# Performance work log

Hardware: AMD Instinct MI355X
Metric: run time of the kernel (lower is better)

Reference implementation:

```python
import jax, jax.numpy as jnp
import numpy as np

NPOINT = 2048

def setup_inputs() -> dict:
    key = jax.random.key(0)
    xyz = jax.random.normal(key, (32, 3, 65536), dtype=jnp.float32)
    return {"xyz": xyz}

def furthest_point_sampling(pts, npoint):
    # pts: [B, N, 3] -> indices [B, npoint] int32
    B, N, _ = pts.shape
    batch = jnp.arange(B)

    def step(carry, _):
        dist, farthest = carry  # dist [B,N], farthest [B]
        centroid = pts[batch, farthest]              # [B, 3]
        d = jnp.sum((pts - centroid[:, None, :]) ** 2, axis=-1)  # [B, N]
        dist = jnp.minimum(dist, d)
        nxt = jnp.argmax(dist, axis=-1).astype(jnp.int32)
        return (dist, nxt), farthest

    init = (jnp.full((B, N), 1e10, dtype=pts.dtype),
            jnp.zeros((B,), dtype=jnp.int32))
    _, idx = jax.lax.scan(step, init, None, length=npoint)
    return idx.T  # [B, npoint]

def reference(xyz):
    # xyz: [B, 3, N]; module permutes to [B, N, 3] and runs FPS
    pts = jnp.transpose(xyz, (0, 2, 1)).astype(jnp.float32)
    return furthest_point_sampling(pts, NPOINT)
```

## Files before the change

kernel.cpp:

```cpp
#include <hip/hip_runtime.h>
#include <stdint.h>

#pragma clang fp contract(off)

#define NPT      2048
#define NBATCH   32
#define NPTS     65536
#define MEMBERS  8
#define NTHREADS 512
#define CHUNK    (NPTS / MEMBERS)
#define PPT      (CHUNK / NTHREADS)
#define WPB      (NTHREADS / 64)
#define PADSLOTS 32

__device__ __forceinline__ uint32_t f2u(float f) { return __float_as_uint(f); }
__device__ __forceinline__ float u2f(uint32_t u) { return __uint_as_float(u); }

__device__ __forceinline__ void amerge(float& v, int& i, float ov, int oi) {
    if (ov > v || (ov == v && oi < i)) { v = ov; i = oi; }
}

template<int CTRL>
__device__ __forceinline__ void dpp_round(float& v, int& i) {
    float ov = u2f((uint32_t)__builtin_amdgcn_mov_dpp((int)f2u(v), CTRL, 0xf, 0xf, true));
    int   oi = __builtin_amdgcn_mov_dpp(i, CTRL, 0xf, 0xf, true);
    amerge(v, i, ov, oi);
}
__device__ __forceinline__ void swz16_round(float& v, int& i) {
    float ov = u2f((uint32_t)__builtin_amdgcn_ds_swizzle((int)f2u(v), 0x401F));
    int   oi = __builtin_amdgcn_ds_swizzle(i, 0x401F);
    amerge(v, i, ov, oi);
}
__device__ __forceinline__ void row16_argmax(float& v, int& i) {
    dpp_round<0xB1>(v, i);
    dpp_round<0x4E>(v, i);
    dpp_round<0x141>(v, i);
    dpp_round<0x140>(v, i);
}
__device__ __forceinline__ void oct_argmax(float& v, int& i) {
    dpp_round<0xB1>(v, i);
    dpp_round<0x4E>(v, i);
    dpp_round<0x141>(v, i);
}

__global__ void __launch_bounds__(NTHREADS)
fps_kernel(const float* __restrict__ xyz, int* __restrict__ out,
           uint64_t* __restrict__ cand)
{
    __shared__ float    sx[CHUNK];
    __shared__ uint64_t red[WPB * 4];
    __shared__ uint32_t bc[4];

    const int i = blockIdx.x;
    const int q = i >> 3;
    const int batch  = (i & 7) * 4 + (q & 3);
    const int member = q >> 2;
    const int tid  = threadIdx.x;
    const int lane = tid & 63;
    const int wv   = tid >> 6;

    const float* xb = xyz + (size_t)batch * 3 * NPTS;
    const int gbase = member * CHUNK;

    float py[PPT], pz[PPT], pd[PPT];
#pragma unroll
    for (int k = 0; k < PPT; ++k) {
        int p = tid + k * NTHREADS;
        int g = gbase + p;
        sx[p] = xb[g];
        py[k] = xb[NPTS + g];
        pz[k] = xb[2 * NPTS + g];
        pd[k] = 1e10f;
    }

    float cx = xb[0], cy = xb[NPTS], cz = xb[2 * NPTS];
    if (member == 0 && tid == 0) out[(size_t)batch * NPT] = 0;

    uint64_t* cb = cand + (size_t)batch * 2 * PADSLOTS;

    for (int t = 0; t < NPT - 1; ++t) {
        float bv = -1.0f;
        int   bi = 0;
#pragma unroll
        for (int k = 0; k < PPT; ++k) {
            int p = tid + k * NTHREADS;
            float dx = sx[p] - cx;
            float dy = py[k] - cy;
            float dz = pz[k] - cz;
            float d  = dx * dx + dy * dy;
            d = d + dz * dz;
            float nd = fminf(pd[k], d);
            pd[k] = nd;
            bool g = nd > bv;
            bv = g ? nd : bv;
            bi = g ? (gbase + p) : bi;
        }

        row16_argmax(bv, bi);
        if ((lane & 15) == 0)
            red[wv * 4 + (lane >> 4)] = ((uint64_t)f2u(bv) << 32) | (uint32_t)bi;
        __syncthreads();

        if (wv == 0) {
            uint64_t c = red[lane & 31];
            float v  = u2f((uint32_t)(c >> 32));
            int   ix = (int)(uint32_t)(c & 0xFFFFFFFFu);
            row16_argmax(v, ix);
            swz16_round(v, ix);

            uint64_t* sb = cb + (size_t)(t & 1) * PADSLOTS;
            const uint32_t tag = (uint32_t)t;
            if (lane == 0) {
                uint64_t w = ((uint64_t)f2u(v) << 32)
                           | ((uint64_t)(uint32_t)ix << 16) | tag;
                __hip_atomic_store(&sb[member], w, __ATOMIC_RELAXED,
                                   __HIP_MEMORY_SCOPE_AGENT);
            }

            uint64_t w = 0; bool done = false;
            do {
                if (!done) w = __hip_atomic_load(&sb[lane & 7], __ATOMIC_RELAXED,
                                                 __HIP_MEMORY_SCOPE_AGENT);
                done = (uint32_t)(w & 0xFFFFu) == tag;
            } while (!__all(done));

            float gv = u2f((uint32_t)(w >> 32));
            int   gi = (int)((w >> 16) & 0xFFFFu);
            oct_argmax(gv, gi);

            float wx = xb[gi], wy = xb[NPTS + gi], wz = xb[2 * NPTS + gi];
            if (lane == 0) {
                bc[0] = f2u(wx); bc[1] = f2u(wy); bc[2] = f2u(wz);
                if (member == 0) out[(size_t)batch * NPT + t + 1] = gi;
            }
        }
        __syncthreads();
        cx = u2f(bc[0]); cy = u2f(bc[1]); cz = u2f(bc[2]);
    }
}

extern "C" void kernel_launch(void* const* d_in, const int* in_sizes, int n_in,
                              void* d_out, int out_size, void* d_ws, size_t ws_size,
                              hipStream_t stream)
{
    const float* xyz = (const float*)d_in[0];
    int* out = (int*)d_out;
    uint64_t* cand = (uint64_t*)d_ws;
    fps_kernel<<<NBATCH * MEMBERS, NTHREADS, 0, stream>>>(xyz, out, cand);
}
```

Before: 4.302 ms.

## Add fast sc0 polling path for cross-block argmax exchange with safe fallback

Each member now writes its candidate twice, once with a plain store to a fast queue and once with an agent-scope atomic store to a safe queue. Waiters poll the fast queue with sc0 loads and fall back to atomic loads of the safe queue after 16 spins, aiming to cut the latency of the per-iteration inter-block handshake. The exchange wave also raises its priority, the local argmax tracks only the slot index k, and the centroid fetch is spread over three lanes. Plain stores and sc0 loads give weaker coherence guarantees across CUs, which is why the fallback path exists.

```diff
diff --git a/kernel.cpp b/kernel.cpp
--- a/kernel.cpp
+++ b/kernel.cpp
@@ -11,7 +11,7 @@
 #define CHUNK    (NPTS / MEMBERS)
 #define PPT      (CHUNK / NTHREADS)
 #define WPB      (NTHREADS / 64)
-#define PADSLOTS 32
+#define LINEPAD  16
 
 __device__ __forceinline__ uint32_t f2u(float f) { return __float_as_uint(f); }
 __device__ __forceinline__ float u2f(uint32_t u) { return __uint_as_float(u); }
@@ -19,7 +19,6 @@
 __device__ __forceinline__ void amerge(float& v, int& i, float ov, int oi) {
     if (ov > v || (ov == v && oi < i)) { v = ov; i = oi; }
 }
-
 template<int CTRL>
 __device__ __forceinline__ void dpp_round(float& v, int& i) {
     float ov = u2f((uint32_t)__builtin_amdgcn_mov_dpp((int)f2u(v), CTRL, 0xf, 0xf, true));
@@ -43,10 +42,25 @@
     dpp_round<0x141>(v, i);
 }
 
+__device__ __forceinline__ uint64_t load_sc0_b64(const uint64_t* p) {
+    uint64_t w;
+    asm volatile("global_load_dwordx2 %0, %1, off sc0\n\t"
+                 "s_waitcnt vmcnt(0)"
+                 : "=v"(w) : "v"(p) : "memory");
+    return w;
+}
+__device__ __forceinline__ void store_plain_b64(uint64_t* p, uint64_t w) {
+    asm volatile("global_store_dwordx2 %0, %1, off"
+                 :: "v"(p), "v"(w) : "memory");
+}
+
 __global__ void __launch_bounds__(NTHREADS)
 fps_kernel(const float* __restrict__ xyz, int* __restrict__ out,
-           uint64_t* __restrict__ cand)
+           uint64_t* __restrict__ ws)
 {
+    uint64_t* fastq = ws;
+    uint64_t* safeq = ws + NBATCH * 2 * LINEPAD;
+
     __shared__ float    sx[CHUNK];
     __shared__ uint64_t red[WPB * 4];
     __shared__ uint32_t bc[4];
@@ -76,11 +90,12 @@
     float cx = xb[0], cy = xb[NPTS], cz = xb[2 * NPTS];
     if (member == 0 && tid == 0) out[(size_t)batch * NPT] = 0;
 
-    uint64_t* cb = cand + (size_t)batch * 2 * PADSLOTS;
+    uint64_t* fb = fastq + (size_t)batch * 2 * LINEPAD;
+    uint64_t* qb = safeq + (size_t)batch * 2 * LINEPAD;
 
     for (int t = 0; t < NPT - 1; ++t) {
         float bv = -1.0f;
-        int   bi = 0;
+        int   bk = 0;
 #pragma unroll
         for (int k = 0; k < PPT; ++k) {
             int p = tid + k * NTHREADS;
@@ -92,9 +107,10 @@
             float nd = fminf(pd[k], d);
             pd[k] = nd;
             bool g = nd > bv;
-            bv = g ? nd : bv;
-            bi = g ? (gbase + p) : bi;
+            bv = fmaxf(bv, nd);
+            bk = g ? k : bk;
         }
+        int bi = gbase + tid + (bk << 9);
 
         row16_argmax(bv, bi);
         if ((lane & 15) == 0)
@@ -102,37 +118,46 @@
         __syncthreads();
 
         if (wv == 0) {
+            __builtin_amdgcn_s_setprio(1);
             uint64_t c = red[lane & 31];
             float v  = u2f((uint32_t)(c >> 32));
             int   ix = (int)(uint32_t)(c & 0xFFFFFFFFu);
             row16_argmax(v, ix);
             swz16_round(v, ix);
 
-            uint64_t* sb = cb + (size_t)(t & 1) * PADSLOTS;
+            uint64_t* sfb = fb + (size_t)(t & 1) * LINEPAD;
+            uint64_t* sqb = qb + (size_t)(t & 1) * LINEPAD;
             const uint32_t tag = (uint32_t)t;
             if (lane == 0) {
                 uint64_t w = ((uint64_t)f2u(v) << 32)
                            | ((uint64_t)(uint32_t)ix << 16) | tag;
-                __hip_atomic_store(&sb[member], w, __ATOMIC_RELAXED,
+                store_plain_b64(&sfb[member], w);
+                __hip_atomic_store(&sqb[member], w, __ATOMIC_RELAXED,
                                    __HIP_MEMORY_SCOPE_AGENT);
             }
 
-            uint64_t w = 0; bool done = false;
+            uint64_t w = 0; bool done = false; int spins = 0;
             do {
-                if (!done) w = __hip_atomic_load(&sb[lane & 7], __ATOMIC_RELAXED,
-                                                 __HIP_MEMORY_SCOPE_AGENT);
-                done = (uint32_t)(w & 0xFFFFu) == tag;
+                if (!done) {
+                    uint64_t wf = load_sc0_b64(&sfb[lane & 7]);
+                    if ((uint32_t)(wf & 0xFFFFu) == tag) { w = wf; done = true; }
+                }
+                if (!done && spins >= 16) {
+                    uint64_t wsf = __hip_atomic_load(&sqb[lane & 7],
+                                                     __ATOMIC_RELAXED,
+                                                     __HIP_MEMORY_SCOPE_AGENT);
+                    if ((uint32_t)(wsf & 0xFFFFu) == tag) { w = wsf; done = true; }
+                }
+                ++spins;
             } while (!__all(done));
 
             float gv = u2f((uint32_t)(w >> 32));
             int   gi = (int)((w >> 16) & 0xFFFFu);
             oct_argmax(gv, gi);
 
-            float wx = xb[gi], wy = xb[NPTS + gi], wz = xb[2 * NPTS + gi];
-            if (lane == 0) {
-                bc[0] = f2u(wx); bc[1] = f2u(wy); bc[2] = f2u(wz);
-                if (member == 0) out[(size_t)batch * NPT + t + 1] = gi;
-            }
+            if (lane < 3) bc[lane] = f2u(xb[(size_t)lane * NPTS + gi]);
+            if (lane == 0 && member == 0) out[(size_t)batch * NPT + t + 1] = gi;
+            __builtin_amdgcn_s_setprio(0);
         }
         __syncthreads();
         cx = u2f(bc[0]); cy = u2f(bc[1]); cz = u2f(bc[2]);
@@ -145,6 +170,6 @@
 {
     const float* xyz = (const float*)d_in[0];
     int* out = (int*)d_out;
-    uint64_t* cand = (uint64_t*)d_ws;
-    fps_kernel<<<NBATCH * MEMBERS, NTHREADS, 0, stream>>>(xyz, out, cand);
+    uint64_t* ws = (uint64_t*)d_ws;
+    fps_kernel<<<NBATCH * MEMBERS, NTHREADS, 0, stream>>>(xyz, out, ws);
 }
```

Result: slower. 7.852 ms (+82.5%).

## Pipeline cross-block candidate polling with prefetched staggered loads and priority boost

Applied to the files above, without the earlier changes.

Replaces the serial spin-wait on the per-batch candidate slots with six prefetched, sleep-staggered system-coherent loads in inline assembly. Each load is checked in turn before the code falls back to the atomic polling loop. It also raises wave priority during the reduction, packs the slot layout more tightly, tracks the local argmax as a loop index instead of a global index, and has three lanes fetch the winner coordinates in parallel. The aim is to cut the latency of the inter-block synchronisation each iteration, at the cost of extra memory traffic and fragile hand-written waitcnt handling.

```diff
diff --git a/kernel.cpp b/kernel.cpp
--- a/kernel.cpp
+++ b/kernel.cpp
@@ -11,7 +11,7 @@
 #define CHUNK    (NPTS / MEMBERS)
 #define PPT      (CHUNK / NTHREADS)
 #define WPB      (NTHREADS / 64)
-#define PADSLOTS 32
+#define LINEPAD  16
 
 __device__ __forceinline__ uint32_t f2u(float f) { return __float_as_uint(f); }
 __device__ __forceinline__ float u2f(uint32_t u) { return __uint_as_float(u); }
@@ -19,7 +19,6 @@
 __device__ __forceinline__ void amerge(float& v, int& i, float ov, int oi) {
     if (ov > v || (ov == v && oi < i)) { v = ov; i = oi; }
 }
-
 template<int CTRL>
 __device__ __forceinline__ void dpp_round(float& v, int& i) {
     float ov = u2f((uint32_t)__builtin_amdgcn_mov_dpp((int)f2u(v), CTRL, 0xf, 0xf, true));
@@ -76,11 +75,11 @@
     float cx = xb[0], cy = xb[NPTS], cz = xb[2 * NPTS];
     if (member == 0 && tid == 0) out[(size_t)batch * NPT] = 0;
 
-    uint64_t* cb = cand + (size_t)batch * 2 * PADSLOTS;
+    uint64_t* cb = cand + (size_t)batch * 2 * LINEPAD;
 
     for (int t = 0; t < NPT - 1; ++t) {
         float bv = -1.0f;
-        int   bi = 0;
+        int   bk = 0;
 #pragma unroll
         for (int k = 0; k < PPT; ++k) {
             int p = tid + k * NTHREADS;
@@ -92,9 +91,10 @@
             float nd = fminf(pd[k], d);
             pd[k] = nd;
             bool g = nd > bv;
-            bv = g ? nd : bv;
-            bi = g ? (gbase + p) : bi;
+            bv = fmaxf(bv, nd);
+            bk = g ? k : bk;
         }
+        int bi = gbase + tid + (bk << 9);
 
         row16_argmax(bv, bi);
         if ((lane & 15) == 0)
@@ -102,13 +102,14 @@
         __syncthreads();
 
         if (wv == 0) {
+            __builtin_amdgcn_s_setprio(1);
             uint64_t c = red[lane & 31];
             float v  = u2f((uint32_t)(c >> 32));
             int   ix = (int)(uint32_t)(c & 0xFFFFFFFFu);
             row16_argmax(v, ix);
             swz16_round(v, ix);
 
-            uint64_t* sb = cb + (size_t)(t & 1) * PADSLOTS;
+            uint64_t* sb = cb + (size_t)(t & 1) * LINEPAD;
             const uint32_t tag = (uint32_t)t;
             if (lane == 0) {
                 uint64_t w = ((uint64_t)f2u(v) << 32)
@@ -117,22 +118,69 @@
                                    __HIP_MEMORY_SCOPE_AGENT);
             }
 
-            uint64_t w = 0; bool done = false;
-            do {
-                if (!done) w = __hip_atomic_load(&sb[lane & 7], __ATOMIC_RELAXED,
-                                                 __HIP_MEMORY_SCOPE_AGENT);
-                done = (uint32_t)(w & 0xFFFFu) == tag;
-            } while (!__all(done));
+            uint64_t* ap = &sb[lane & 7];
+            uint64_t s0, s1, s2, s3, s4, s5;
+            asm volatile(
+                "s_sleep 3\n\t"
+                "global_load_dwordx2 %0, %6, off sc1\n\t"
+                "s_sleep 2\n\t"
+                "global_load_dwordx2 %1, %6, off sc1\n\t"
+                "s_sleep 2\n\t"
+                "global_load_dwordx2 %2, %6, off sc1\n\t"
+                "s_sleep 2\n\t"
+                "global_load_dwordx2 %3, %6, off sc1\n\t"
+                "s_sleep 2\n\t"
+                "global_load_dwordx2 %4, %6, off sc1\n\t"
+                "s_sleep 2\n\t"
+                "global_load_dwordx2 %5, %6, off sc1\n\t"
+                "s_waitcnt vmcnt(5)"
+                : "=&v"(s0), "=&v"(s1), "=&v"(s2), "=&v"(s3), "=&v"(s4), "=&v"(s5)
+                : "v"(ap)
+                : "memory");
+
+            uint64_t w = s0;
+            bool done = (uint32_t)(s0 & 0xFFFFu) == tag;
+            if (!__all(done)) {
+                asm volatile("s_waitcnt vmcnt(4)" : "+v"(s1));
+                bool m = (uint32_t)(s1 & 0xFFFFu) == tag;
+                if (!done && m) { w = s1; done = true; }
+                if (!__all(done)) {
+                    asm volatile("s_waitcnt vmcnt(3)" : "+v"(s2));
+                    m = (uint32_t)(s2 & 0xFFFFu) == tag;
+                    if (!done && m) { w = s2; done = true; }
+                    if (!__all(done)) {
+                        asm volatile("s_waitcnt vmcnt(2)" : "+v"(s3));
+                        m = (uint32_t)(s3 & 0xFFFFu) == tag;
+                        if (!done && m) { w = s3; done = true; }
+                        if (!__all(done)) {
+                            asm volatile("s_waitcnt vmcnt(1)" : "+v"(s4));
+                            m = (uint32_t)(s4 & 0xFFFFu) == tag;
+                            if (!done && m) { w = s4; done = true; }
+                            if (!__all(done)) {
+                                asm volatile("s_waitcnt vmcnt(0)" : "+v"(s5));
+                                m = (uint32_t)(s5 & 0xFFFFu) == tag;
+                                if (!done && m) { w = s5; done = true; }
+                            }
+                        }
+                    }
+                }
+            }
+            while (!__all(done)) {
+                uint64_t x = __hip_atomic_load(ap, __ATOMIC_RELAXED,
+                                               __HIP_MEMORY_SCOPE_AGENT);
+                if (!done && (uint32_t)(x & 0xFFFFu) == tag) { w = x; done = true; }
+            }
 
             float gv = u2f((uint32_t)(w >> 32));
             int   gi = (int)((w >> 16) & 0xFFFFu);
             oct_argmax(gv, gi);
 
-            float wx = xb[gi], wy = xb[NPTS + gi], wz = xb[2 * NPTS + gi];
-            if (lane == 0) {
-                bc[0] = f2u(wx); bc[1] = f2u(wy); bc[2] = f2u(wz);
-                if (member == 0) out[(size_t)batch * NPT + t + 1] = gi;
-            }
+            if (lane < 3) bc[lane] = f2u(xb[(size_t)lane * NPTS + gi]);
+            if (lane == 0 && member == 0) out[(size_t)batch * NPT + t + 1] = gi;
+
+            asm volatile("s_waitcnt vmcnt(0)"
+                         :: "v"(s1), "v"(s2), "v"(s3), "v"(s4), "v"(s5));
+            __builtin_amdgcn_s_setprio(0);
         }
         __syncthreads();
         cx = u2f(bc[0]); cy = u2f(bc[1]); cz = u2f(bc[2]);
```

Measured after the change: 4.572 ms. +6.3%, slower.

## Interleave two batches per block to hide cross-block sync latency

Applied to the files above, without the earlier changes.

Each block now processes two batches, A and B, over a chunk half as large, with 16 members per batch instead of 8. The cross-block poll for one batch's winner runs while the distance update for the other batch executes, so the global atomic handshake latency is overlapped with compute. The in-thread argmax also tracks a loop index instead of a global index. In exchange, each thread holds twice as many register arrays, every iteration needs more barriers, and twice as many blocks take part in each spin-wait group.

```diff
diff --git a/kernel.cpp b/kernel.cpp
--- a/kernel.cpp
+++ b/kernel.cpp
@@ -6,12 +6,13 @@
 #define NPT      2048
 #define NBATCH   32
 #define NPTS     65536
-#define MEMBERS  8
+#define MEMBERS  16
+#define NGROUPS  (NBATCH / 2)
 #define NTHREADS 512
 #define CHUNK    (NPTS / MEMBERS)
 #define PPT      (CHUNK / NTHREADS)
 #define WPB      (NTHREADS / 64)
-#define PADSLOTS 32
+#define LINEPAD  32
 
 __device__ __forceinline__ uint32_t f2u(float f) { return __float_as_uint(f); }
 __device__ __forceinline__ float u2f(uint32_t u) { return __uint_as_float(u); }
@@ -19,7 +20,6 @@
 __device__ __forceinline__ void amerge(float& v, int& i, float ov, int oi) {
     if (ov > v || (ov == v && oi < i)) { v = ov; i = oi; }
 }
-
 template<int CTRL>
 __device__ __forceinline__ void dpp_round(float& v, int& i) {
     float ov = u2f((uint32_t)__builtin_amdgcn_mov_dpp((int)f2u(v), CTRL, 0xf, 0xf, true));
@@ -37,105 +37,154 @@
     dpp_round<0x141>(v, i);
     dpp_round<0x140>(v, i);
 }
-__device__ __forceinline__ void oct_argmax(float& v, int& i) {
-    dpp_round<0xB1>(v, i);
-    dpp_round<0x4E>(v, i);
-    dpp_round<0x141>(v, i);
+
+__device__ __forceinline__ void reduce_publish(const uint64_t* red, uint64_t* sb,
+                                               uint32_t tag, int lane, int member) {
+    uint64_t c = red[lane & 31];
+    float v  = u2f((uint32_t)(c >> 32));
+    int   ix = (int)(uint32_t)(c & 0xFFFFFFFFu);
+    row16_argmax(v, ix);
+    swz16_round(v, ix);
+    if (lane == 0) {
+        uint64_t w = ((uint64_t)f2u(v) << 32)
+                   | ((uint64_t)(uint32_t)ix << 16) | tag;
+        __hip_atomic_store(&sb[member], w, __ATOMIC_RELAXED,
+                           __HIP_MEMORY_SCOPE_AGENT);
+    }
 }
+
+__device__ __forceinline__ void poll_line(const uint64_t* sb, uint32_t tag,
+                                          int lane, float& gv, int& gi) {
+    uint64_t w = 0; bool done = false;
+    do {
+        if (!done) w = __hip_atomic_load(&sb[lane & 15], __ATOMIC_RELAXED,
+                                         __HIP_MEMORY_SCOPE_AGENT);
+        done = (uint32_t)(w & 0xFFFFu) == tag;
+    } while (!__all(done));
+    gv = u2f((uint32_t)(w >> 32));
+    gi = (int)((w >> 16) & 0xFFFFu);
+    row16_argmax(gv, gi);
+}
+
+#define COMPUTE_PHASE(sx, py, pz, pd, bc, red)                              \
+    {                                                                       \
+        float cx = u2f(bc[0]), cy = u2f(bc[1]), cz = u2f(bc[2]);            \
+        float bv = -1.0f; int bk = 0;                                       \
+        _Pragma("unroll")                                                   \
+        for (int k = 0; k < PPT; ++k) {                                     \
+            int p = tid + k * NTHREADS;                                     \
+            float dx = sx[p] - cx;                                          \
+            float dy = py[k] - cy;                                          \
+            float dz = pz[k] - cz;                                          \
+            float d  = dx * dx + dy * dy;   \
+            d = d + dz * dz;                    \
+            float nd = fminf(pd[k], d);                                     \
+            pd[k] = nd;                                                     \
+            bool g = nd > bv;                                               \
+            bv = fmaxf(bv, nd);                                             \
+            bk = g ? k : bk;                                                \
+        }                                                                   \
+        int bi = gbase + tid + (bk << 9);                                   \
+        row16_argmax(bv, bi);                                               \
+        if ((lane & 15) == 0)                                               \
+            red[wv * 4 + (lane >> 4)] =                                     \
+                ((uint64_t)f2u(bv) << 32) | (uint32_t)bi;                   \
+    }
 
 __global__ void __launch_bounds__(NTHREADS)
 fps_kernel(const float* __restrict__ xyz, int* __restrict__ out,
            uint64_t* __restrict__ cand)
 {
-    __shared__ float    sx[CHUNK];
-    __shared__ uint64_t red[WPB * 4];
-    __shared__ uint32_t bc[4];
+    __shared__ float    sxA[CHUNK], sxB[CHUNK];
+    __shared__ uint64_t redA[32], redB[32];
+    __shared__ uint32_t bcA[4], bcB[4];
 
     const int i = blockIdx.x;
-    const int q = i >> 3;
-    const int batch  = (i & 7) * 4 + (q & 3);
-    const int member = q >> 2;
+    const int member = i >> 4;
+    const int group  = i & 15;
+    const int batchA = group * 2;
+    const int batchB = group * 2 + 1;
     const int tid  = threadIdx.x;
     const int lane = tid & 63;
     const int wv   = tid >> 6;
 
-    const float* xb = xyz + (size_t)batch * 3 * NPTS;
+    const float* xbA = xyz + (size_t)batchA * 3 * NPTS;
+    const float* xbB = xyz + (size_t)batchB * 3 * NPTS;
     const int gbase = member * CHUNK;
 
-    float py[PPT], pz[PPT], pd[PPT];
+    float pyA[PPT], pzA[PPT], pdA[PPT];
+    float pyB[PPT], pzB[PPT], pdB[PPT];
 #pragma unroll
     for (int k = 0; k < PPT; ++k) {
         int p = tid + k * NTHREADS;
         int g = gbase + p;
-        sx[p] = xb[g];
-        py[k] = xb[NPTS + g];
-        pz[k] = xb[2 * NPTS + g];
-        pd[k] = 1e10f;
+        sxA[p] = xbA[g];
+        pyA[k] = xbA[NPTS + g];
+        pzA[k] = xbA[2 * NPTS + g];
+        pdA[k] = 1e10f;
+        sxB[p] = xbB[g];
+        pyB[k] = xbB[NPTS + g];
+        pzB[k] = xbB[2 * NPTS + g];
+        pdB[k] = 1e10f;
     }
 
-    float cx = xb[0], cy = xb[NPTS], cz = xb[2 * NPTS];
-    if (member == 0 && tid == 0) out[(size_t)batch * NPT] = 0;
+    if (tid == 0) {
+        bcA[0] = f2u(xbA[0]); bcA[1] = f2u(xbA[NPTS]); bcA[2] = f2u(xbA[2 * NPTS]);
+        bcB[0] = f2u(xbB[0]); bcB[1] = f2u(xbB[NPTS]); bcB[2] = f2u(xbB[2 * NPTS]);
+        if (member == 0) {
+            out[(size_t)batchA * NPT] = 0;
+            out[(size_t)batchB * NPT] = 0;
+        }
+    }
+    __syncthreads();
 
-    uint64_t* cb = cand + (size_t)batch * 2 * PADSLOTS;
+    uint64_t* cbA = cand + (size_t)batchA * 2 * LINEPAD;
+    uint64_t* cbB = cand + (size_t)batchB * 2 * LINEPAD;
 
     for (int t = 0; t < NPT - 1; ++t) {
-        float bv = -1.0f;
-        int   bi = 0;
-#pragma unroll
-        for (int k = 0; k < PPT; ++k) {
-            int p = tid + k * NTHREADS;
-            float dx = sx[p] - cx;
-            float dy = py[k] - cy;
-            float dz = pz[k] - cz;
-            float d  = dx * dx + dy * dy;
-            d = d + dz * dz;
-            float nd = fminf(pd[k], d);
-            pd[k] = nd;
-            bool g = nd > bv;
-            bv = g ? nd : bv;
-            bi = g ? (gbase + p) : bi;
-        }
+        const uint32_t tag = (uint32_t)t;
 
-        row16_argmax(bv, bi);
-        if ((lane & 15) == 0)
-            red[wv * 4 + (lane >> 4)] = ((uint64_t)f2u(bv) << 32) | (uint32_t)bi;
+        COMPUTE_PHASE(sxA, pyA, pzA, pdA, bcA, redA);
         __syncthreads();
 
         if (wv == 0) {
-            uint64_t c = red[lane & 31];
-            float v  = u2f((uint32_t)(c >> 32));
-            int   ix = (int)(uint32_t)(c & 0xFFFFFFFFu);
-            row16_argmax(v, ix);
-            swz16_round(v, ix);
-
-            uint64_t* sb = cb + (size_t)(t & 1) * PADSLOTS;
-            const uint32_t tag = (uint32_t)t;
-            if (lane == 0) {
-                uint64_t w = ((uint64_t)f2u(v) << 32)
-                           | ((uint64_t)(uint32_t)ix << 16) | tag;
-                __hip_atomic_store(&sb[member], w, __ATOMIC_RELAXED,
-                                   __HIP_MEMORY_SCOPE_AGENT);
-            }
-
-            uint64_t w = 0; bool done = false;
-            do {
-                if (!done) w = __hip_atomic_load(&sb[lane & 7], __ATOMIC_RELAXED,
-                                                 __HIP_MEMORY_SCOPE_AGENT);
-                done = (uint32_t)(w & 0xFFFFu) == tag;
-            } while (!__all(done));
-
-            float gv = u2f((uint32_t)(w >> 32));
-            int   gi = (int)((w >> 16) & 0xFFFFu);
-            oct_argmax(gv, gi);
-
-            float wx = xb[gi], wy = xb[NPTS + gi], wz = xb[2 * NPTS + gi];
-            if (lane == 0) {
-                bc[0] = f2u(wx); bc[1] = f2u(wy); bc[2] = f2u(wz);
-                if (member == 0) out[(size_t)batch * NPT + t + 1] = gi;
-            }
+            __builtin_amdgcn_s_setprio(1);
+            reduce_publish(redA, cbA + (size_t)(t & 1) * LINEPAD, tag, lane, member);
+            __builtin_amdgcn_s_setprio(0);
+        } else if (wv == 1 && t > 0) {
+            __builtin_amdgcn_s_setprio(1);
+            float gv; int gi;
+            poll_line(cbB + (size_t)((t - 1) & 1) * LINEPAD, (uint32_t)(t - 1),
+                      lane, gv, gi);
+            if (lane < 3) bcB[lane] = f2u(xbB[(size_t)lane * NPTS + gi]);
+            if (lane == 0 && member == 0) out[(size_t)batchB * NPT + t] = gi;
+            __builtin_amdgcn_s_setprio(0);
         }
         __syncthreads();
-        cx = u2f(bc[0]); cy = u2f(bc[1]); cz = u2f(bc[2]);
+
+        COMPUTE_PHASE(sxB, pyB, pzB, pdB, bcB, redB);
+        __syncthreads();
+
+        if (wv == 0) {
+            __builtin_amdgcn_s_setprio(1);
+            reduce_publish(redB, cbB + (size_t)(t & 1) * LINEPAD, tag, lane, member);
+            __builtin_amdgcn_s_setprio(0);
+        } else if (wv == 1) {
+            __builtin_amdgcn_s_setprio(1);
+            float gv; int gi;
+            poll_line(cbA + (size_t)(t & 1) * LINEPAD, tag, lane, gv, gi);
+            if (lane < 3) bcA[lane] = f2u(xbA[(size_t)lane * NPTS + gi]);
+            if (lane == 0 && member == 0) out[(size_t)batchA * NPT + t + 1] = gi;
+            __builtin_amdgcn_s_setprio(0);
+        }
+        __syncthreads();
+    }
+
+    if (member == 0 && wv == 1) {
+        const uint32_t tag = NPT - 2;
+        float gv; int gi;
+        poll_line(cbB + (size_t)(tag & 1) * LINEPAD, tag, lane, gv, gi);
+        if (lane == 0) out[(size_t)batchB * NPT + NPT - 1] = gi;
     }
 }
 
@@ -146,5 +195,5 @@
     const float* xyz = (const float*)d_in[0];
     int* out = (int*)d_out;
     uint64_t* cand = (uint64_t*)d_ws;
-    fps_kernel<<<NBATCH * MEMBERS, NTHREADS, 0, stream>>>(xyz, out, cand);
+    fps_kernel<<<NGROUPS * MEMBERS, NTHREADS, 0, stream>>>(xyz, out, cand);
 }
```

Result: slower. 5.565 ms (+29.4%).
